# Kernel tuning notes

Hardware: AMD Instinct MI355X
Metric: run time of the kernel (lower is better)

## Reference

```python
import jax, jax.numpy as jnp
import numpy as np

B, S, D, H = 2, 2048, 1024, 16
DK = D // H


def setup_inputs() -> dict:
    key = jax.random.key(0)
    ks = jax.random.split(key, 11)
    scale = 1.0 / np.sqrt(D)
    inp = {
        'q': jax.random.normal(ks[0], (B, S, D), jnp.float32),
        'k': jax.random.normal(ks[1], (B, S, D), jnp.float32),
        'v': jax.random.normal(ks[2], (B, S, D), jnp.float32),
        'mask': jnp.tril(jnp.ones((S, S), jnp.int32))[None, None],  # [1,1,S,S] causal
        'w_q': jax.random.normal(ks[3], (D, D), jnp.float32) * scale,
        'b_q': jax.random.normal(ks[4], (D,), jnp.float32) * scale,
        'w_k': jax.random.normal(ks[5], (D, D), jnp.float32) * scale,
        'b_k': jax.random.normal(ks[6], (D,), jnp.float32) * scale,
        'w_v': jax.random.normal(ks[7], (D, D), jnp.float32) * scale,
        'b_v': jax.random.normal(ks[8], (D,), jnp.float32) * scale,
        'w_o': jax.random.normal(ks[9], (D, D), jnp.float32) * scale,
        'b_o': jax.random.normal(ks[10], (D,), jnp.float32) * scale,
    }
    return inp


def reference(q, k, v, mask, w_q, b_q, w_k, b_k, w_v, b_v, w_o, b_o):
    # Linear projections (torch Linear: x @ W^T + b; here weights stored as [D_in, D_out])
    query = q @ w_q + b_q  # [B,S,D]
    key_ = k @ w_k + b_k
    value = v @ w_v + b_v
    # split heads -> [B,H,S,DK]
    def split(x):
        return x.reshape(B, S, H, DK).transpose(0, 2, 1, 3)
    qh, kh, vh = split(query), split(key_), split(value)
    scores = jnp.einsum('bhqd,bhkd->bhqk', qh, kh) / jnp.sqrt(jnp.float32(DK))
    scores = jnp.where(mask == 0, jnp.float32(-1e9), scores)
    attn = jax.nn.softmax(scores, axis=-1)  # dropout p=0.0 -> identity
    out = jnp.einsum('bhqk,bhkd->bhqd', attn, vh)  # [B,H,S,DK]
    out = out.transpose(0, 2, 1, 3).reshape(B, S, D)
    return out @ w_o + b_o
```

## Files before the change

kernel.cpp:

```cpp
#include <hip/hip_runtime.h>

typedef unsigned short u16;
typedef unsigned int u32;
typedef __attribute__((ext_vector_type(8))) short short8;
typedef __attribute__((ext_vector_type(4))) float f32x4;
typedef __attribute__((ext_vector_type(16))) float f32x16;
typedef __attribute__((ext_vector_type(4))) float float4v;
typedef __attribute__((ext_vector_type(4))) u16 u16x4;

#define DEV static __device__ __forceinline__

static constexpr int S_LEN = 2048;
static constexpr int D_MODEL = 1024;
static constexpr int N_HEADS = 16;
static constexpr int DK = 64;
static constexpr float LOG2E = 1.4426950408889634f;
static constexpr float SM_SHIFT = 12.0f;

#if defined(__has_builtin)
#if __has_builtin(__builtin_amdgcn_exp2f)
#define EXP2(x) __builtin_amdgcn_exp2f(x)
#else
#define EXP2(x) exp2f(x)
#endif
#else
#define EXP2(x) exp2f(x)
#endif

DEV u16 f2bf(float f) {
  u32 u = __builtin_bit_cast(u32, f);
  u32 r = (u + 0x7FFFu + ((u >> 16) & 1u)) >> 16;
  return (u16)r;
}

DEV u32 pk2bf(float lo, float hi) {
  u32 d;
  asm("v_cvt_pk_bf16_f32 %0, %1, %2" : "=v"(d) : "v"(lo), "v"(hi));
  return d;
}

DEV void swap32(u32& a, u32& b) {
  asm volatile("v_permlane32_swap_b32 %0, %1" : "+v"(a), "+v"(b));
}

DEV short8 mk8(u32 w0, u32 w1, u32 w2, u32 w3) {
  union { u32 u[4]; short8 s; } t;
  t.u[0] = w0; t.u[1] = w1; t.u[2] = w2; t.u[3] = w3;
  return t.s;
}

DEV void async16(const void* g, void* l) {
  __builtin_amdgcn_global_load_lds(
      (const __attribute__((address_space(1))) u32*)g,
      (__attribute__((address_space(3))) u32*)l, 16, 0, 0);
}

DEV short8 lds_frag(const u16* tile, int row, int byteInRow) {
  const char* p = (const char*)tile + row * 128 + (byteInRow ^ ((row & 7) << 4));
  return *(const short8*)p;
}

DEV f32x4 mfma16(short8 a, short8 b, f32x4 c) {
  return __builtin_amdgcn_mfma_f32_16x16x32_bf16(a, b, c, 0, 0, 0);
}

DEV f32x16 mfma32(short8 a, short8 b, f32x16 c) {
  return __builtin_amdgcn_mfma_f32_32x32x16_bf16(a, b, c, 0, 0, 0);
}

__global__ void k_prep(const float* __restrict__ q, const float* __restrict__ k,
                       const float* __restrict__ v,
                       const float* __restrict__ wq, const float* __restrict__ wk,
                       const float* __restrict__ wv, const float* __restrict__ wo,
                       u16* __restrict__ xq, u16* __restrict__ xk, u16* __restrict__ xv,
                       u16* __restrict__ tq, u16* __restrict__ tk,
                       u16* __restrict__ tv, u16* __restrict__ to_) {
  __shared__ u16 t[64][65];
  const int z = blockIdx.y;
  if (z < 3) {
    const float* src = z == 0 ? q : (z == 1 ? k : v);
    u16* dst = z == 0 ? xq : (z == 1 ? xk : xv);
    int i = (blockIdx.x * 256 + threadIdx.x) * 4;
    const int stride = 512 * 256 * 4;
    for (; i < 4096 * 1024; i += stride) {
      float4v f = *(const float4v*)(src + i);
      u16x4 o;
      o[0] = f2bf(f[0]); o[1] = f2bf(f[1]); o[2] = f2bf(f[2]); o[3] = f2bf(f[3]);
      *(u16x4*)(dst + i) = o;
    }
  } else {
    if (blockIdx.x >= 256) return;
    const int zz = z - 3;
    const float* W = zz == 0 ? wq : (zz == 1 ? wk : (zz == 2 ? wv : wo));
    u16* Wt = zz == 0 ? tq : (zz == 1 ? tk : (zz == 2 ? tv : to_));
    const int n0 = (blockIdx.x & 15) * 64;
    const int k0 = (blockIdx.x >> 4) * 64;
    const int tid = threadIdx.x;
    const int c = tid & 63, r0 = tid >> 6;
#pragma unroll
    for (int j = 0; j < 16; ++j) {
      int r = r0 + j * 4;
      t[r][c] = f2bf(W[(size_t)(k0 + r) * D_MODEL + n0 + c]);
    }
    __syncthreads();
#pragma unroll
    for (int j = 0; j < 16; ++j) {
      int r = r0 + j * 4;
      Wt[(size_t)(n0 + r) * D_MODEL + k0 + c] = t[c][r];
    }
  }
}

__global__ __launch_bounds__(256, 3) void k_gemm3(
    const u16* __restrict__ Xq, const u16* __restrict__ Xk, const u16* __restrict__ Xv,
    const u16* __restrict__ Wtq, const u16* __restrict__ Wtk, const u16* __restrict__ Wtv,
    const float* __restrict__ bq, const float* __restrict__ bk, const float* __restrict__ bv,
    u16* __restrict__ Qh, u16* __restrict__ Kh, u16* __restrict__ Vtp) {
  const int lin = blockIdx.x + (blockIdx.y << 5) + (blockIdx.z << 8);
  const int wg = (lin & 7) * 96 + (lin >> 3);
  const int bx = wg & 31, by = (wg >> 5) & 7;
  const int z = wg >> 8;
  const u16* A = z == 0 ? Xq : (z == 1 ? Xk : Xv);
  const u16* Bt = z == 0 ? Wtq : (z == 1 ? Wtk : Wtv);
  const float* bias = z == 0 ? bq : (z == 1 ? bk : bv);
  u16* obf = z == 0 ? Qh : (z == 1 ? Kh : Vtp);
  const float scale = z == 0 ? 0.125f * LOG2E : 1.0f;

  __shared__ __align__(16) u16 As[128 * 64];
  __shared__ __align__(16) u16 Bs[128 * 64];
  const int tid = threadIdx.x;
  const int lane = tid & 63, w = tid >> 6;
  const int l15 = lane & 15, l4 = lane >> 4;
  const int bm = bx * 128, bn = by * 128;
  const int wr = (w >> 1) * 64, wc = (w & 1) * 64;
  const int sr = tid >> 3, sc8 = tid & 7;
  f32x4 acc[4][4] = {};

  for (int k0 = 0; k0 < 1024; k0 += 64) {
    __syncthreads();
#pragma unroll
    for (int j = 0; j < 4; ++j) {
      int row = sr + j * 32;
      int col = (sc8 ^ (row & 7)) << 3;
      async16(A + (size_t)(bm + row) * 1024 + k0 + col, (char*)As + tid * 16 + j * 4096);
      async16(Bt + (size_t)(bn + row) * 1024 + k0 + col, (char*)Bs + tid * 16 + j * 4096);
    }
    __syncthreads();
    short8 af[4][2], bfv[4][2];
#pragma unroll
    for (int mi = 0; mi < 4; ++mi)
#pragma unroll
      for (int kk = 0; kk < 2; ++kk)
        af[mi][kk] = lds_frag(As, wr + mi * 16 + l15, kk * 64 + l4 * 16);
#pragma unroll
    for (int ni = 0; ni < 4; ++ni)
#pragma unroll
      for (int kk = 0; kk < 2; ++kk)
        bfv[ni][kk] = lds_frag(Bs, wc + ni * 16 + l15, kk * 64 + l4 * 16);
#pragma unroll
    for (int kk = 0; kk < 2; ++kk)
#pragma unroll
      for (int mi = 0; mi < 4; ++mi)
#pragma unroll
        for (int ni = 0; ni < 4; ++ni)
          acc[mi][ni] = mfma16(af[mi][kk], bfv[ni][kk], acc[mi][ni]);
  }

#pragma unroll
  for (int mi = 0; mi < 4; ++mi)
#pragma unroll
    for (int ni = 0; ni < 4; ++ni) {
      const int row0 = bm + wr + mi * 16 + l4 * 4;
      const int col = bn + wc + ni * 16 + l15;
      const int h = col >> 6, dk = col & 63;
      const int b = row0 >> 11, s0 = row0 & 2047;
      if (z == 2) {
        u16x4 pk;
#pragma unroll
        for (int r = 0; r < 4; ++r) pk[r] = f2bf(acc[mi][ni][r] + bias[col]);
        *(u16x4*)(obf + ((size_t)((b * N_HEADS + h) * DK + dk)) * S_LEN + s0) = pk;
      } else {
#pragma unroll
        for (int r = 0; r < 4; ++r) {
          float vv = (acc[mi][ni][r] + bias[col]) * scale;
          obf[(((size_t)(b * N_HEADS + h) * S_LEN + s0 + r) << 6) + dk] = f2bf(vv);
        }
      }
    }
}

__global__ __launch_bounds__(256, 3) void k_gemmO(
    const u16* __restrict__ A, const u16* __restrict__ Bt,
    const float* __restrict__ bias, float* __restrict__ ofp) {
  const int lin = blockIdx.x + (blockIdx.y << 5);
  const int wg = (lin & 7) * 64 + (lin >> 3);
  const int bx = wg & 31, by = wg >> 5;
  __shared__ __align__(16) u16 As[128 * 64];
  __shared__ __align__(16) u16 Bs[64 * 64];
  const int tid = threadIdx.x;
  const int lane = tid & 63, w = tid >> 6;
  const int l15 = lane & 15, l4 = lane >> 4;
  const int bm = bx * 128, bn = by * 64;
  const int wr = w * 32;
  const int sr = tid >> 3, sc8 = tid & 7;
  f32x4 acc[2][4] = {};

  for (int k0 = 0; k0 < 1024; k0 += 64) {
    __syncthreads();
#pragma unroll
    for (int j = 0; j < 4; ++j) {
      int row = sr + j * 32;
      int col = (sc8 ^ (row & 7)) << 3;
      async16(A + (size_t)(bm + row) * 1024 + k0 + col, (char*)As + tid * 16 + j * 4096);
      if (j < 2)
        async16(Bt + (size_t)(bn + row) * 1024 + k0 + col, (char*)Bs + tid * 16 + j * 4096);
    }
    __syncthreads();
    short8 af[2][2], bfv[4][2];
#pragma unroll
    for (int mi = 0; mi < 2; ++mi)
#pragma unroll
      for (int kk = 0; kk < 2; ++kk)
        af[mi][kk] = lds_frag(As, wr + mi * 16 + l15, kk * 64 + l4 * 16);
#pragma unroll
    for (int ni = 0; ni < 4; ++ni)
#pragma unroll
      for (int kk = 0; kk < 2; ++kk)
        bfv[ni][kk] = lds_frag(Bs, ni * 16 + l15, kk * 64 + l4 * 16);
#pragma unroll
    for (int kk = 0; kk < 2; ++kk)
#pragma unroll
      for (int mi = 0; mi < 2; ++mi)
#pragma unroll
        for (int ni = 0; ni < 4; ++ni)
          acc[mi][ni] = mfma16(af[mi][kk], bfv[ni][kk], acc[mi][ni]);
  }

#pragma unroll
  for (int mi = 0; mi < 2; ++mi)
#pragma unroll
    for (int ni = 0; ni < 4; ++ni)
#pragma unroll
      for (int r = 0; r < 4; ++r) {
        int row = bm + wr + mi * 16 + l4 * 4 + r;
        int col = bn + ni * 16 + l15;
        ofp[(size_t)row * D_MODEL + col] = acc[mi][ni][r] + bias[col];
      }
}

__global__ __launch_bounds__(256, 4) void k_attn(
    const u16* __restrict__ Qh, const u16* __restrict__ Kh,
    const u16* __restrict__ Vt, u16* __restrict__ Om) {
  __shared__ __align__(16) u16 Ks[2][64 * 64];
  __shared__ __align__(16) u16 Vs[2][64 * 64];
  const int tid = threadIdx.x;
  const int lane = tid & 63, w = tid >> 6;
  const int l31 = lane & 31, hf = (lane >> 5) & 1;
  const int qh = w & 1, kvh = w >> 1;
  const int bh = blockIdx.x;
  const int y = blockIdx.y, y0 = y & 7, qd = y >> 3;
  const int jq = qd == 0 ? y0 : (qd == 1 ? 31 - y0 : (qd == 2 ? 8 + y0 : 23 - y0));
  const int q0 = jq * 64;
  const int qw = q0 + qh * 32;
  const u16* Qb = Qh + (size_t)bh * S_LEN * DK;
  const u16* Kb = Kh + (size_t)bh * S_LEN * DK;
  const u16* Vb = Vt + (size_t)bh * DK * S_LEN;
  const int sc8 = tid & 7;
  const int b = bh >> 4, hd = bh & 15;

  auto stage = [&](int t0, int buf) {
#pragma unroll
    for (int j = 0; j < 2; ++j) {
      int row = (tid >> 3) + j * 32;
      int col = (sc8 ^ (row & 7)) << 3;
      async16(Kb + (size_t)(t0 + row) * DK + col, (char*)Ks[buf] + tid * 16 + j * 4096);
      async16(Vb + (size_t)row * S_LEN + t0 + col, (char*)Vs[buf] + tid * 16 + j * 4096);
    }
  };

  short8 qB[4];
#pragma unroll
  for (int cc = 0; cc < 4; ++cc)
    qB[cc] = *(const short8*)(Qb + (size_t)(qw + l31) * DK + cc * 16 + hf * 8);

  f32x16 od0, od1;
#pragma unroll
  for (int r = 0; r < 16; ++r) { od0[r] = 0.f; od1[r] = 0.f; }
  float rs = 0.f;
  const int nt = jq + 1;

  stage(0, 0);
  __syncthreads();
  int cur = 0;
#pragma unroll 1
  for (int ti = 0; ti < nt; ++ti) {
    const int t0 = ti << 6;
    if (ti + 1 < nt) stage(t0 + 64, cur ^ 1);

    f32x16 s;
#pragma unroll
    for (int r = 0; r < 16; ++r) s[r] = -SM_SHIFT;
    __builtin_amdgcn_s_setprio(1);
#pragma unroll
    for (int cc = 0; cc < 4; ++cc) {
      short8 kf = lds_frag(Ks[cur], kvh * 32 + l31, cc * 32 + hf * 16);
      s = mfma32(kf, qB[cc], s);
    }
    __builtin_amdgcn_s_setprio(0);

    if (t0 + kvh * 32 + 31 > qw) {
      const int qrow = qw + l31;
#pragma unroll
      for (int r = 0; r < 16; ++r) {
        int kr = t0 + kvh * 32 + ((r & 3) + 8 * (r >> 2) + 4 * hf);
        if (kr > qrow) s[r] = -1e30f;
      }
    }

#pragma unroll
    for (int r = 0; r < 16; ++r) s[r] = EXP2(s[r]);
    {
      float t01 = (s[0] + s[1]) + (s[2] + s[3]);
      float t23 = (s[4] + s[5]) + (s[6] + s[7]);
      float t45 = (s[8] + s[9]) + (s[10] + s[11]);
      float t67 = (s[12] + s[13]) + (s[14] + s[15]);
      rs += (t01 + t23) + (t45 + t67);
    }

    u32 a0 = pk2bf(s[0], s[1]), b0 = pk2bf(s[4], s[5]);
    u32 c0 = pk2bf(s[2], s[3]), d0 = pk2bf(s[6], s[7]);
    swap32(a0, b0); swap32(c0, d0);
    short8 pbA = mk8(a0, c0, b0, d0);
    u32 e0 = pk2bf(s[8], s[9]), f0 = pk2bf(s[12], s[13]);
    u32 g0 = pk2bf(s[10], s[11]), h0 = pk2bf(s[14], s[15]);
    swap32(e0, f0); swap32(g0, h0);
    short8 pbB = mk8(e0, g0, f0, h0);

    __builtin_amdgcn_s_setprio(1);
    {
      short8 v00 = lds_frag(Vs[cur], l31, kvh * 64 + hf * 16);
      short8 v10 = lds_frag(Vs[cur], 32 + l31, kvh * 64 + hf * 16);
      od0 = mfma32(v00, pbA, od0);
      od1 = mfma32(v10, pbA, od1);
      short8 v01 = lds_frag(Vs[cur], l31, kvh * 64 + 32 + hf * 16);
      short8 v11 = lds_frag(Vs[cur], 32 + l31, kvh * 64 + 32 + hf * 16);
      od0 = mfma32(v01, pbB, od0);
      od1 = mfma32(v11, pbB, od1);
    }
    __builtin_amdgcn_s_setprio(0);
    __syncthreads();
    cur ^= 1;
  }

  rs += __shfl_xor(rs, 32);

  float* cb = (float*)Ks;
  float* cr = (float*)Vs;
  if (kvh == 0) {
    float4v* dv = (float4v*)cb + ((qh * 64 + lane) * 8);
#pragma unroll
    for (int rr = 0; rr < 4; ++rr) {
      float4v v0, v1;
#pragma unroll
      for (int i = 0; i < 4; ++i) { v0[i] = od0[rr * 4 + i]; v1[i] = od1[rr * 4 + i]; }
      dv[rr] = v0;
      dv[4 + rr] = v1;
    }
    cr[qh * 64 + lane] = rs;
  }
  __syncthreads();
  if (kvh == 1) {
    const float4v* dv = (const float4v*)cb + ((qh * 64 + lane) * 8);
#pragma unroll
    for (int rr = 0; rr < 4; ++rr) {
      float4v v0 = dv[rr], v1 = dv[4 + rr];
#pragma unroll
      for (int i = 0; i < 4; ++i) {
        od0[rr * 4 + i] += v0[i];
        od1[rr * 4 + i] += v1[i];
      }
    }
    rs += cr[qh * 64 + lane];
    const float inv = 1.f / rs;
    u16* dst = Om + (size_t)(b * S_LEN + qw + l31) * D_MODEL + hd * DK;
#pragma unroll
    for (int rr = 0; rr < 4; ++rr) {
      u16x4 o0, o1;
#pragma unroll
      for (int i = 0; i < 4; ++i) {
        o0[i] = f2bf(od0[rr * 4 + i] * inv);
        o1[i] = f2bf(od1[rr * 4 + i] * inv);
      }
      *(u16x4*)(dst + rr * 8 + 4 * hf) = o0;
      *(u16x4*)(dst + 32 + rr * 8 + 4 * hf) = o1;
    }
  }
}

extern "C" void kernel_launch(void* const* d_in, const int* in_sizes, int n_in,
                              void* d_out, int out_size, void* d_ws, size_t ws_size,
                              hipStream_t stream) {
  (void)in_sizes; (void)n_in; (void)out_size; (void)ws_size;
  const float* q  = (const float*)d_in[0];
  const float* k  = (const float*)d_in[1];
  const float* v  = (const float*)d_in[2];
  const float* wq = (const float*)d_in[4];
  const float* bq = (const float*)d_in[5];
  const float* wk = (const float*)d_in[6];
  const float* bk = (const float*)d_in[7];
  const float* wv = (const float*)d_in[8];
  const float* bv = (const float*)d_in[9];
  const float* wo = (const float*)d_in[10];
  const float* bo = (const float*)d_in[11];
  float* out = (float*)d_out;

  char* ws = (char*)d_ws;
  const size_t XB = (size_t)4096 * 1024 * 2;
  const size_t WB = (size_t)1024 * 1024 * 2;
  u16* Xq  = (u16*)(ws);
  u16* Xk  = (u16*)(ws + XB);
  u16* Xv  = (u16*)(ws + 2 * XB);
  u16* Wtq = (u16*)(ws + 3 * XB);
  u16* Wtk = (u16*)(ws + 3 * XB + WB);
  u16* Wtv = (u16*)(ws + 3 * XB + 2 * WB);
  u16* Wto = (u16*)(ws + 3 * XB + 3 * WB);
  u16* Qh  = (u16*)(ws + 3 * XB + 4 * WB);
  u16* Kh  = (u16*)(ws + 4 * XB + 4 * WB);
  u16* Vtp = (u16*)(ws + 5 * XB + 4 * WB);
  u16* Om  = Xq;

  k_prep<<<dim3(512, 7), 256, 0, stream>>>(q, k, v, wq, wk, wv, wo,
                                           Xq, Xk, Xv, Wtq, Wtk, Wtv, Wto);
  k_gemm3<<<dim3(32, 8, 3), 256, 0, stream>>>(Xq, Xk, Xv, Wtq, Wtk, Wtv,
                                              bq, bk, bv, Qh, Kh, Vtp);
  k_attn<<<dim3(32, 32), 256, 0, stream>>>(Qh, Kh, Vtp, Om);
  k_gemmO<<<dim3(32, 16), 256, 0, stream>>>(Om, Wto, bo, out);
}
```

Before: 104.9 us.

## Give each wave private K/V LDS buffers and drop per-tile block barriers

```diff
diff --git a/kernel.cpp b/kernel.cpp
--- a/kernel.cpp
+++ b/kernel.cpp
@@ -248,11 +248,11 @@
       }
 }
 
-__global__ __launch_bounds__(256, 4) void k_attn(
+__global__ __launch_bounds__(256, 2) void k_attn(
     const u16* __restrict__ Qh, const u16* __restrict__ Kh,
     const u16* __restrict__ Vt, u16* __restrict__ Om) {
-  __shared__ __align__(16) u16 Ks[2][64 * 64];
-  __shared__ __align__(16) u16 Vs[2][64 * 64];
+  __shared__ __align__(16) u16 KV[4][2][4096];
+  __shared__ float crs[128];
   const int tid = threadIdx.x;
   const int lane = tid & 63, w = tid >> 6;
   const int l31 = lane & 31, hf = (lane >> 5) & 1;
@@ -265,16 +265,22 @@
   const u16* Qb = Qh + (size_t)bh * S_LEN * DK;
   const u16* Kb = Kh + (size_t)bh * S_LEN * DK;
   const u16* Vb = Vt + (size_t)bh * DK * S_LEN;
-  const int sc8 = tid & 7;
   const int b = bh >> 4, hd = bh & 15;
 
   auto stage = [&](int t0, int buf) {
-#pragma unroll
-    for (int j = 0; j < 2; ++j) {
-      int row = (tid >> 3) + j * 32;
-      int col = (sc8 ^ (row & 7)) << 3;
-      async16(Kb + (size_t)(t0 + row) * DK + col, (char*)Ks[buf] + tid * 16 + j * 4096);
-      async16(Vb + (size_t)row * S_LEN + t0 + col, (char*)Vs[buf] + tid * 16 + j * 4096);
+    char* kb = (char*)&KV[w][buf][0];
+    char* vb = (char*)&KV[w][buf][2048];
+    const int r8 = lane >> 3, c8 = lane & 7;
+#pragma unroll
+    for (int j = 0; j < 4; ++j) {
+      int row = j * 8 + r8;
+      int lk = c8 ^ (row & 7);
+      async16(Kb + (size_t)(t0 + kvh * 32 + row) * DK + lk * 8,
+              kb + j * 1024 + lane * 16);
+      int dk = row + (lk >> 2) * 32;
+      int soff = (lk & 3) * 8;
+      async16(Vb + (size_t)dk * S_LEN + t0 + kvh * 32 + soff,
+              vb + j * 1024 + lane * 16);
     }
   };
 
@@ -282,6 +288,8 @@
 #pragma unroll
   for (int cc = 0; cc < 4; ++cc)
     qB[cc] = *(const short8*)(Qb + (size_t)(qw + l31) * DK + cc * 16 + hf * 8);
+  __builtin_amdgcn_s_waitcnt(0);
+  __builtin_amdgcn_sched_barrier(0);
 
   f32x16 od0, od1;
 #pragma unroll
@@ -290,12 +298,19 @@
   const int nt = jq + 1;
 
   stage(0, 0);
-  __syncthreads();
   int cur = 0;
 #pragma unroll 1
   for (int ti = 0; ti < nt; ++ti) {
     const int t0 = ti << 6;
-    if (ti + 1 < nt) stage(t0 + 64, cur ^ 1);
+    if (ti + 1 < nt) {
+      stage(t0 + 64, cur ^ 1);
+      asm volatile("s_waitcnt vmcnt(8)" ::: "memory");
+    } else {
+      asm volatile("s_waitcnt vmcnt(0)" ::: "memory");
+    }
+    __builtin_amdgcn_sched_barrier(0);
+    const u16* Kw = &KV[w][cur][0];
+    const u16* Vw = &KV[w][cur][2048];
 
     f32x16 s;
 #pragma unroll
@@ -303,7 +318,7 @@
     __builtin_amdgcn_s_setprio(1);
 #pragma unroll
     for (int cc = 0; cc < 4; ++cc) {
-      short8 kf = lds_frag(Ks[cur], kvh * 32 + l31, cc * 32 + hf * 16);
+      short8 kf = lds_frag(Kw, l31, cc * 32 + hf * 16);
       s = mfma32(kf, qB[cc], s);
     }
     __builtin_amdgcn_s_setprio(0);
@@ -338,26 +353,24 @@
 
     __builtin_amdgcn_s_setprio(1);
     {
-      short8 v00 = lds_frag(Vs[cur], l31, kvh * 64 + hf * 16);
-      short8 v10 = lds_frag(Vs[cur], 32 + l31, kvh * 64 + hf * 16);
+      short8 v00 = lds_frag(Vw, l31, hf * 16);
+      short8 v10 = lds_frag(Vw, l31, 64 + hf * 16);
       od0 = mfma32(v00, pbA, od0);
       od1 = mfma32(v10, pbA, od1);
-      short8 v01 = lds_frag(Vs[cur], l31, kvh * 64 + 32 + hf * 16);
-      short8 v11 = lds_frag(Vs[cur], 32 + l31, kvh * 64 + 32 + hf * 16);
+      short8 v01 = lds_frag(Vw, l31, 32 + hf * 16);
+      short8 v11 = lds_frag(Vw, l31, 96 + hf * 16);
       od0 = mfma32(v01, pbB, od0);
       od1 = mfma32(v11, pbB, od1);
     }
     __builtin_amdgcn_s_setprio(0);
-    __syncthreads();
     cur ^= 1;
   }
 
   rs += __shfl_xor(rs, 32);
 
-  float* cb = (float*)Ks;
-  float* cr = (float*)Vs;
+  __syncthreads();
   if (kvh == 0) {
-    float4v* dv = (float4v*)cb + ((qh * 64 + lane) * 8);
+    float4v* dv = (float4v*)((char*)KV + (size_t)w * 16384) + lane * 8;
 #pragma unroll
     for (int rr = 0; rr < 4; ++rr) {
       float4v v0, v1;
@@ -366,11 +379,11 @@
       dv[rr] = v0;
       dv[4 + rr] = v1;
     }
-    cr[qh * 64 + lane] = rs;
+    crs[qh * 64 + lane] = rs;
   }
   __syncthreads();
   if (kvh == 1) {
-    const float4v* dv = (const float4v*)cb + ((qh * 64 + lane) * 8);
+    const float4v* dv = (const float4v*)((char*)KV + (size_t)(w - 2) * 16384) + lane * 8;
 #pragma unroll
     for (int rr = 0; rr < 4; ++rr) {
       float4v v0 = dv[rr], v1 = dv[4 + rr];
@@ -380,7 +393,7 @@
         od1[rr * 4 + i] += v1[i];
       }
     }
-    rs += cr[qh * 64 + lane];
+    rs += crs[qh * 64 + lane];
     const float inv = 1.f / rs;
     u16* dst = Om + (size_t)(b * S_LEN + qw + l31) * D_MODEL + hd * DK;
 #pragma unroll
```

Result: slower. 112.2 us (+6.9%).

## Enlarge attention blocks to 128 queries with 8 waves sharing K/V tiles

Applied to the files above, without the earlier changes.

```diff
diff --git a/kernel.cpp b/kernel.cpp
--- a/kernel.cpp
+++ b/kernel.cpp
@@ -248,20 +248,21 @@
       }
 }
 
-__global__ __launch_bounds__(256, 4) void k_attn(
+__global__ __launch_bounds__(512, 4) void k_attn(
     const u16* __restrict__ Qh, const u16* __restrict__ Kh,
     const u16* __restrict__ Vt, u16* __restrict__ Om) {
   __shared__ __align__(16) u16 Ks[2][64 * 64];
   __shared__ __align__(16) u16 Vs[2][64 * 64];
+  __shared__ float crs[256];
   const int tid = threadIdx.x;
   const int lane = tid & 63, w = tid >> 6;
   const int l31 = lane & 31, hf = (lane >> 5) & 1;
-  const int qh = w & 1, kvh = w >> 1;
+  const int qq = w & 3, kvh = w >> 2;
   const int bh = blockIdx.x;
-  const int y = blockIdx.y, y0 = y & 7, qd = y >> 3;
-  const int jq = qd == 0 ? y0 : (qd == 1 ? 31 - y0 : (qd == 2 ? 8 + y0 : 23 - y0));
-  const int q0 = jq * 64;
-  const int qw = q0 + qh * 32;
+  const int m = blockIdx.y;
+  const int g = m < 8 ? m : 23 - m;
+  const int q0 = g * 128;
+  const int qw = q0 + qq * 32;
   const u16* Qb = Qh + (size_t)bh * S_LEN * DK;
   const u16* Kb = Kh + (size_t)bh * S_LEN * DK;
   const u16* Vb = Vt + (size_t)bh * DK * S_LEN;
@@ -269,13 +270,10 @@
   const int b = bh >> 4, hd = bh & 15;
 
   auto stage = [&](int t0, int buf) {
-#pragma unroll
-    for (int j = 0; j < 2; ++j) {
-      int row = (tid >> 3) + j * 32;
-      int col = (sc8 ^ (row & 7)) << 3;
-      async16(Kb + (size_t)(t0 + row) * DK + col, (char*)Ks[buf] + tid * 16 + j * 4096);
-      async16(Vb + (size_t)row * S_LEN + t0 + col, (char*)Vs[buf] + tid * 16 + j * 4096);
-    }
+    int row = tid >> 3;
+    int col = (sc8 ^ (row & 7)) << 3;
+    async16(Kb + (size_t)(t0 + row) * DK + col, (char*)Ks[buf] + tid * 16);
+    async16(Vb + (size_t)row * S_LEN + t0 + col, (char*)Vs[buf] + tid * 16);
   };
 
   short8 qB[4];
@@ -287,7 +285,7 @@
 #pragma unroll
   for (int r = 0; r < 16; ++r) { od0[r] = 0.f; od1[r] = 0.f; }
   float rs = 0.f;
-  const int nt = jq + 1;
+  const int nt = 2 * g + 2;
 
   stage(0, 0);
   __syncthreads();
@@ -354,10 +352,9 @@
 
   rs += __shfl_xor(rs, 32);
 
-  float* cb = (float*)Ks;
-  float* cr = (float*)Vs;
   if (kvh == 0) {
-    float4v* dv = (float4v*)cb + ((qh * 64 + lane) * 8);
+    float* base = (qq < 2) ? (float*)Ks + qq * 2048 : (float*)Vs + (qq - 2) * 2048;
+    float4v* dv = (float4v*)base + lane * 8;
 #pragma unroll
     for (int rr = 0; rr < 4; ++rr) {
       float4v v0, v1;
@@ -366,11 +363,12 @@
       dv[rr] = v0;
       dv[4 + rr] = v1;
     }
-    cr[qh * 64 + lane] = rs;
+    crs[qq * 64 + lane] = rs;
   }
   __syncthreads();
   if (kvh == 1) {
-    const float4v* dv = (const float4v*)cb + ((qh * 64 + lane) * 8);
+    const float* base = (qq < 2) ? (float*)Ks + qq * 2048 : (float*)Vs + (qq - 2) * 2048;
+    const float4v* dv = (const float4v*)base + lane * 8;
 #pragma unroll
     for (int rr = 0; rr < 4; ++rr) {
       float4v v0 = dv[rr], v1 = dv[4 + rr];
@@ -380,7 +378,7 @@
         od1[rr * 4 + i] += v1[i];
       }
     }
-    rs += cr[qh * 64 + lane];
+    rs += crs[qq * 64 + lane];
     const float inv = 1.f / rs;
     u16* dst = Om + (size_t)(b * S_LEN + qw + l31) * D_MODEL + hd * DK;
 #pragma unroll
@@ -433,6 +431,6 @@
                                            Xq, Xk, Xv, Wtq, Wtk, Wtv, Wto);
   k_gemm3<<<dim3(32, 8, 3), 256, 0, stream>>>(Xq, Xk, Xv, Wtq, Wtk, Wtv,
                                               bq, bk, bv, Qh, Kh, Vtp);
-  k_attn<<<dim3(32, 32), 256, 0, stream>>>(Qh, Kh, Vtp, Om);
+  k_attn<<<dim3(32, 16), 512, 0, stream>>>(Qh, Kh, Vtp, Om);
   k_gemmO<<<dim3(32, 16), 256, 0, stream>>>(Om, Wto, bo, out);
 }
```

Result: slower. 108.9 us (+3.8%).
